# Performance work log

Measured on AMD Instinct MI355X. Metric: run time of the kernel, lower is better.

The kernel has to match this reference:

```python
import jax, jax.numpy as jnp
import numpy as np

# Hard-coded constants from the original module
GAMMA = 0.1      # self.gamma default
N_STEPS = 10     # self.n_steps default
RHO = 0.9        # RMSProp decay
LR = 0.009       # RMSProp learning rate
MOM = 0.9        # momentum
EPS = 1e-8       # RMSProp epsilon
ABS_EPS = 1e-6   # diff_abs smoothing: diff_abs(x) = sqrt(x^2 + 1e-6)

B, IN_DIM, OUT_DIM = 4096, 2048, 4096


def setup_inputs() -> dict:
    key = jax.random.key(0)
    k1, k2 = jax.random.split(key)
    inputs = jax.random.normal(k1, (B, IN_DIM), dtype=jnp.float32)
    # keras 'uniform' init: U(-0.05, 0.05), shape (output_dim, input_dim)
    W = jax.random.uniform(k2, (OUT_DIM, IN_DIM), minval=-0.05, maxval=0.05, dtype=jnp.float32)
    return {"inputs": inputs, "W": W}


def reference(inputs, W):
    batch = inputs.shape[0]
    out_dim = W.shape[0]
    a = jnp.sqrt(inputs * inputs + ABS_EPS)          # diff_abs(inputs), [B, in_dim]
    act = lambda u: 0.5 * (1.0 + jnp.exp(-u))        # self.activation

    def cost(x):
        # l1_norm.sum() + l1_inov + own_norm  (prior = 0)
        l1 = (GAMMA * act(x @ W) * a).sum()
        l1_inov = (GAMMA / 10.0) * jnp.sum(x * x)
        own = GAMMA * jnp.sum(jnp.sqrt(x * x + ABS_EPS))
        return l1 + l1_inov + own

    grad_cost = jax.grad(cost)

    def step(carry, _):
        x, acc1, acc2 = carry
        g = grad_cost(x)                              # [B, out_dim]
        new_acc1 = RHO * acc1 + (1.0 - RHO) * g * g
        denom = jnp.sqrt(new_acc1 + EPS)
        new_acc2 = MOM * acc2 - LR * g / denom
        cand = x - LR * g / denom
        t = 0.1 * LR / denom                          # elementwise prox threshold
        new_x = jnp.maximum(cand - t, 0.0) + jnp.minimum(cand + t, 0.0) + MOM * new_acc2
        new_x = jax.lax.stop_gradient(new_x)          # theano disconnected_grad
        return (new_x, new_acc1, new_acc2), None

    z = jnp.zeros((batch, out_dim), dtype=inputs.dtype)
    # scan runs n_steps; last step's l1_norm uses the state after n_steps-1 updates,
    # so run n_steps-1 updates then compute the final l1_norm directly.
    (x, _, _), _ = jax.lax.scan(step, (z, z, z), None, length=N_STEPS - 1)
    return GAMMA * act(x @ W) * a                     # outputs[-1][-1]: last l1_norm, [B, in_dim]
```

## Files before the change

### kernel.cpp

```cpp
#include <hip/hip_runtime.h>
#include <cstdint>
#include <cstddef>

#define B_DIM   4096
#define IN_DIM  2048
#define OUT_DIM 4096

typedef __attribute__((ext_vector_type(8))) __bf16 bf16x8;
typedef __attribute__((ext_vector_type(4))) float  f32x4;
typedef unsigned short ushortT;

__device__ __forceinline__ ushortT f2bf(float f) {
    unsigned int u = __float_as_uint(f);
    u += 0x7FFFu + ((u >> 16) & 1u);
    return (ushortT)(u >> 16);
}
__device__ __forceinline__ float bf2f(ushortT b) {
    return __uint_as_float(((unsigned int)b) << 16);
}

__device__ __forceinline__ void gload16(const void* g, void* l) {
    __builtin_amdgcn_global_load_lds(
        (const __attribute__((address_space(1))) void*)g,
        (__attribute__((address_space(3))) void*)l, 16, 0, 0);
}

__global__ void prep_g0_kernel(const float* __restrict__ in, ushortT* __restrict__ Gb) {
    int i = blockIdx.x * 256 + threadIdx.x;
    float4 v = reinterpret_cast<const float4*>(in)[i];
    ushort4 g;
    g.x = f2bf(-0.05f * sqrtf(v.x * v.x + 1e-6f));
    g.y = f2bf(-0.05f * sqrtf(v.y * v.y + 1e-6f));
    g.z = f2bf(-0.05f * sqrtf(v.z * v.z + 1e-6f));
    g.w = f2bf(-0.05f * sqrtf(v.w * v.w + 1e-6f));
    reinterpret_cast<ushort4*>(Gb)[i] = g;
}

__global__ void conv_w_kernel(const float* __restrict__ W, ushortT* __restrict__ Wb,
                              ushortT* __restrict__ WTb) {
    __shared__ float tile[64][65];
    const int i0 = blockIdx.x * 64;
    const int j0 = blockIdx.y * 64;
    const int c  = threadIdx.x & 63;
    const int rq = threadIdx.x >> 6;
#pragma unroll
    for (int rp = 0; rp < 16; ++rp) {
        int row = rp * 4 + rq;
        float w = W[(size_t)(j0 + row) * IN_DIM + i0 + c];
        tile[row][c] = w;
        Wb[(size_t)(j0 + row) * IN_DIM + i0 + c] = f2bf(w);
    }
    __syncthreads();
#pragma unroll
    for (int rp = 0; rp < 16; ++rp) {
        int row = rp * 4 + rq;
        WTb[(size_t)(i0 + row) * OUT_DIM + j0 + c] = f2bf(tile[c][row]);
    }
}

#define EPILOGUE(MR_)                                                          \
    float* lep = (float*)(smem + w * 4352);                                    \
    const int li = lane >> 4;                                                  \
    const int lc = lane & 15;                                                  \
    _Pragma("unroll")                                                          \
    for (int m = 0; m < (MR_); ++m) {                                          \
        _Pragma("unroll")                                                      \
        for (int n = 0; n < 4; ++n)                                            \
            _Pragma("unroll")                                                  \
            for (int i = 0; i < 4; ++i)                                        \
                lep[(li * 4 + i) * 68 + n * 16 + lc] = acc[m][n][i];           \
        asm volatile("s_waitcnt lgkmcnt(0)" ::: "memory");                     \
        __builtin_amdgcn_sched_barrier(0);                                     \
        _Pragma("unroll")                                                      \
        for (int rr = 0; rr < 4; ++rr) {                                       \
            const int row = rr + li * 4;                                       \
            float4 v = *reinterpret_cast<const float4*>(&lep[row * 68 + lc * 4]); \
            const size_t idx  = (size_t)(row0w + m * 16 + row) * N + col0w + lc * 4; \
            const size_t idx4 = idx >> 2;                                      \
            if constexpr (EPI == 0) {                                          \
                float4 iv = reinterpret_cast<const float4*>(inb)[idx4];        \
                ushort4 g;                                                     \
                g.x = f2bf(-0.05f * sqrtf(iv.x * iv.x + 1e-6f) * expf(-v.x));  \
                g.y = f2bf(-0.05f * sqrtf(iv.y * iv.y + 1e-6f) * expf(-v.y));  \
                g.z = f2bf(-0.05f * sqrtf(iv.z * iv.z + 1e-6f) * expf(-v.z));  \
                g.w = f2bf(-0.05f * sqrtf(iv.w * iv.w + 1e-6f) * expf(-v.w));  \
                *reinterpret_cast<ushort4*>(&Gb[idx]) = g;                     \
            } else if constexpr (EPI == 1) {                                   \
                float4 iv = reinterpret_cast<const float4*>(inb)[idx4];        \
                float4 o;                                                      \
                o.x = 0.05f * (1.0f + expf(-v.x)) * sqrtf(iv.x * iv.x + 1e-6f); \
                o.y = 0.05f * (1.0f + expf(-v.y)) * sqrtf(iv.y * iv.y + 1e-6f); \
                o.z = 0.05f * (1.0f + expf(-v.z)) * sqrtf(iv.z * iv.z + 1e-6f); \
                o.w = 0.05f * (1.0f + expf(-v.w)) * sqrtf(iv.w * iv.w + 1e-6f); \
                reinterpret_cast<float4*>(out)[idx4] = o;                      \
            } else {                                                           \
                ushort4 xu  = *reinterpret_cast<const ushort4*>(&xb[idx]);     \
                ushort4 a1u = *reinterpret_cast<const ushort4*>(&acc1[idx]);   \
                ushort4 a2u = *reinterpret_cast<const ushort4*>(&acc2[idx]);   \
                float xs[4] = {bf2f(xu.x), bf2f(xu.y), bf2f(xu.z), bf2f(xu.w)}; \
                float vs[4] = {v.x, v.y, v.z, v.w};                            \
                ushortT a1s[4] = {a1u.x, a1u.y, a1u.z, a1u.w};                 \
                ushortT a2s[4] = {a2u.x, a2u.y, a2u.z, a2u.w};                 \
                ushortT a1n[4], a2n[4], xbn[4];                                \
                _Pragma("unroll")                                              \
                for (int j = 0; j < 4; ++j) {                                  \
                    float g    = vs[j] + 0.02f * xs[j] + 0.1f * xs[j] * rsqrtf(xs[j] * xs[j] + 1e-6f); \
                    float a1   = 0.9f * bf2f(a1s[j]) + 0.1f * g * g;           \
                    float inv  = rsqrtf(a1 + 1e-8f);                           \
                    float r_   = 0.009f * g * inv;                             \
                    float a2   = 0.9f * bf2f(a2s[j]) - r_;                     \
                    float cand = xs[j] - r_;                                   \
                    float t_   = 0.0009f * inv;                                \
                    float xn   = fmaxf(cand - t_, 0.0f) + fminf(cand + t_, 0.0f) + 0.9f * a2; \
                    a1n[j] = f2bf(a1); a2n[j] = f2bf(a2); xbn[j] = f2bf(xn);   \
                }                                                              \
                *reinterpret_cast<ushort4*>(&acc1[idx]) = make_ushort4(a1n[0], a1n[1], a1n[2], a1n[3]); \
                *reinterpret_cast<ushort4*>(&acc2[idx]) = make_ushort4(a2n[0], a2n[1], a2n[2], a2n[3]); \
                *reinterpret_cast<ushort4*>(&xb[idx])   = make_ushort4(xbn[0], xbn[1], xbn[2], xbn[3]); \
            }                                                                  \
        }                                                                      \
        asm volatile("s_waitcnt lgkmcnt(0)" ::: "memory");                     \
    }

#define PHASE(MB, RB, SLOTP, STTILE, C0, NC)                                   \
    {                                                                          \
        const char* sb_ = (SLOTP);                                             \
        if (RB) {                                                              \
            _Pragma("unroll")                                                  \
            for (int n = 0; n < 4; ++n)                                        \
                bF[n] = *reinterpret_cast<const bf16x8*>(sb_ + bRd[n]);        \
        }                                                                      \
        bf16x8 aF[4];                                                          \
        _Pragma("unroll")                                                      \
        for (int m = 0; m < 4; ++m)                                            \
            aF[m] = *reinterpret_cast<const bf16x8*>(sb_ + aRd[m]);            \
        if ((STTILE) < nt) {                                                   \
            _Pragma("unroll")                                                  \
            for (int c = 0; c < (NC); ++c) stage_chunk((STTILE), (C0) + c);    \
        }                                                                      \
        __builtin_amdgcn_sched_barrier(0);                                     \
        __builtin_amdgcn_s_barrier();                                          \
        asm volatile("s_waitcnt lgkmcnt(0)" ::: "memory");                     \
        __builtin_amdgcn_sched_barrier(0);                                     \
        __builtin_amdgcn_s_setprio(1);                                         \
        _Pragma("unroll")                                                      \
        for (int m = 0; m < 4; ++m) {                                          \
            _Pragma("unroll")                                                  \
            for (int n = 0; n < 4; ++n)                                        \
                acc[m][n] = __builtin_amdgcn_mfma_f32_16x16x32_bf16(           \
                    aF[m], bF[n], acc[m][n], 0, 0, 0);                         \
        }                                                                      \
        __builtin_amdgcn_s_setprio(0);                                         \
        __builtin_amdgcn_s_barrier();                                          \
        __builtin_amdgcn_sched_barrier(0);                                     \
    }

template <int EPI>
__global__ __launch_bounds__(512, 1)
void gemm_phase(const ushortT* __restrict__ A, const ushortT* __restrict__ Bm,
                int N, int K,
                const float* __restrict__ inb, ushortT* __restrict__ Gb,
                float* __restrict__ out,
                ushortT* __restrict__ acc1, ushortT* __restrict__ acc2,
                ushortT* __restrict__ xb) {
    constexpr int BM = 128, BN = 256;
    constexpr int ASZ  = BM * 64;
    constexpr int SLOT = ASZ + BN * 64;
    constexpr int LA   = 1, LB = 2, L = 3;
    __shared__ alignas(16) char smem[4 * SLOT];

    const int tid  = threadIdx.x;
    const int lane = tid & 63;
    const int w    = tid >> 6;
    const int wm   = w >> 2;
    const int wn   = w & 3;
    const int nbx  = N / BN;
    const int nwg  = gridDim.x;
    const int cpx  = nwg >> 3;
    const int bid  = (int)blockIdx.x;
    const int swz  = (bid & 7) * cpx + (bid >> 3);
    const int bx   = swz % nbx;
    const int by   = swz / nbx;
    const int row0 = by * BM;
    const int col0 = bx * BN;
    const size_t strideK2 = (size_t)K * 2;

    const char* gp[L]; int lo[L];
#pragma unroll
    for (int i = 0; i < LA; ++i) {
        int Lp  = i * 512 + tid;
        int row = Lp >> 2, sl = Lp & 3;
        int src = sl ^ ((row >> 1) & 3);
        gp[i] = (const char*)A + (size_t)(row0 + row) * strideK2 + src * 16;
        lo[i] = i * 8192 + w * 1024;
    }
#pragma unroll
    for (int i = 0; i < LB; ++i) {
        int Lp  = i * 512 + tid;
        int row = Lp >> 2, sl = Lp & 3;
        int src = sl ^ ((row >> 1) & 3);
        gp[LA + i] = (const char*)Bm + (size_t)(col0 + row) * strideK2 + src * 16;
        lo[LA + i] = ASZ + i * 8192 + w * 1024;
    }
    auto stage_all = [&](int tt) {
        char* sb = smem + (tt & 3) * SLOT;
        const size_t kb = (size_t)tt * 64;
#pragma unroll
        for (int c = 0; c < L; ++c) gload16(gp[c] + kb, sb + lo[c]);
    };
    auto stage_chunk = [&](int tt, int c) {
        gload16(gp[c] + (size_t)tt * 64, smem + (tt & 3) * SLOT + lo[c]);
    };

    int aRd[4], bRd[4];
#pragma unroll
    for (int m = 0; m < 4; ++m) {
        int row = wm * 64 + m * 16 + (lane & 15);
        aRd[m] = row * 64 + (((lane >> 4) ^ ((row >> 1) & 3)) * 16);
    }
#pragma unroll
    for (int n = 0; n < 4; ++n) {
        int row = wn * 64 + n * 16 + (lane & 15);
        bRd[n] = ASZ + row * 64 + (((lane >> 4) ^ ((row >> 1) & 3)) * 16);
    }

    f32x4 acc[4][4] = {};
    const int nt = K >> 5;

    stage_all(0); stage_all(1); stage_all(2);

    for (int tt = 0; tt < nt; tt += 2) {
        if (tt + 2 < nt) asm volatile("s_waitcnt vmcnt(%0)" :: "n"(L) : "memory");
        else             asm volatile("s_waitcnt vmcnt(0)"  ::: "memory");
        __builtin_amdgcn_s_barrier();
        __builtin_amdgcn_sched_barrier(0);

        const char* sb0 = smem + (tt & 3) * SLOT;
        const char* sb1 = smem + ((tt + 1) & 3) * SLOT;
        bf16x8 bF[4];
        PHASE(0, true, sb0, tt + 3, 0, 3)
        PHASE(0, true, sb1, tt + 4, 0, 3)
    }

    __builtin_amdgcn_s_barrier();
    const int row0w = row0 + wm * 64;
    const int col0w = col0 + wn * 64;
    EPILOGUE(4)
}

template <int EPI>
__global__ __launch_bounds__(512, 4)
void gemm_mb2(const ushortT* __restrict__ A, const ushortT* __restrict__ Bm,
              int N, int K,
              const float* __restrict__ inb, ushortT* __restrict__ Gb,
              float* __restrict__ out,
              ushortT* __restrict__ acc1, ushortT* __restrict__ acc2,
              ushortT* __restrict__ xb) {
    constexpr int BM = 256, BN = 128;
    constexpr int ASZ  = BM * 64;
    constexpr int SLOT = ASZ + BN * 64;
    constexpr int CA   = 2, CB = 1, L = 3;
    __shared__ alignas(16) char smem[2 * SLOT];

    const int tid  = threadIdx.x;
    const int lane = tid & 63;
    const int w    = tid >> 6;
    const int wm   = w >> 1;
    const int wn   = w & 1;
    const int nbx  = N / BN;
    const int nwg  = gridDim.x;
    const int cpx  = nwg >> 3;
    const int bid  = (int)blockIdx.x;
    const int swz  = (bid & 7) * cpx + (bid >> 3);
    const int bx   = swz % nbx;
    const int by   = swz / nbx;
    const int row0 = by * BM;
    const int col0 = bx * BN;
    const size_t strideK2 = (size_t)K * 2;

    const char* gp[L]; int lo[L];
#pragma unroll
    for (int c = 0; c < CA; ++c) {
        int Lp  = c * 512 + tid;
        int row = Lp >> 2, sl = Lp & 3;
        int src = sl ^ ((row >> 1) & 3);
        gp[c] = (const char*)A + (size_t)(row0 + row) * strideK2 + src * 16;
        lo[c] = c * 8192 + w * 1024;
    }
#pragma unroll
    for (int c = 0; c < CB; ++c) {
        int Lp  = c * 512 + tid;
        int row = Lp >> 2, sl = Lp & 3;
        int src = sl ^ ((row >> 1) & 3);
        gp[CA + c] = (const char*)Bm + (size_t)(col0 + row) * strideK2 + src * 16;
        lo[CA + c] = ASZ + c * 8192 + w * 1024;
    }
    auto stage = [&](int tt) {
        char* sb = smem + (tt & 1) * SLOT;
        const size_t kb = (size_t)tt * 64;
#pragma unroll
        for (int c = 0; c < L; ++c) gload16(gp[c] + kb, sb + lo[c]);
    };

    int aRd[4], bRd[4];
#pragma unroll
    for (int m = 0; m < 4; ++m) {
        int row = wm * 64 + m * 16 + (lane & 15);
        aRd[m] = row * 64 + (((lane >> 4) ^ ((row >> 1) & 3)) * 16);
    }
#pragma unroll
    for (int n = 0; n < 4; ++n) {
        int row = wn * 64 + n * 16 + (lane & 15);
        bRd[n] = ASZ + row * 64 + (((lane >> 4) ^ ((row >> 1) & 3)) * 16);
    }

    f32x4 acc[4][4] = {};
    const int nt = K >> 5;

    stage(0);

    for (int tt = 0; tt < nt; ++tt) {
        asm volatile("s_waitcnt vmcnt(0)" ::: "memory");
        __builtin_amdgcn_s_barrier();
        __builtin_amdgcn_sched_barrier(0);

        const char* sb = smem + (tt & 1) * SLOT;
        bf16x8 aF[4], bF[4];
#pragma unroll
        for (int n = 0; n < 4; ++n) bF[n] = *reinterpret_cast<const bf16x8*>(sb + bRd[n]);
#pragma unroll
        for (int m = 0; m < 4; ++m) aF[m] = *reinterpret_cast<const bf16x8*>(sb + aRd[m]);
        if (tt + 1 < nt) stage(tt + 1);
        __builtin_amdgcn_s_setprio(1);
#pragma unroll
        for (int m = 0; m < 4; ++m)
#pragma unroll
            for (int n = 0; n < 4; ++n)
                acc[m][n] = __builtin_amdgcn_mfma_f32_16x16x32_bf16(aF[m], bF[n], acc[m][n], 0, 0, 0);
        __builtin_amdgcn_s_setprio(0);
    }

    __builtin_amdgcn_s_barrier();
    const int row0w = row0 + wm * 64;
    const int col0w = col0 + wn * 64;
    EPILOGUE(4)
}

extern "C" void kernel_launch(void* const* d_in, const int* in_sizes, int n_in,
                              void* d_out, int out_size, void* d_ws, size_t ws_size,
                              hipStream_t stream) {
    const float* in = (const float*)d_in[0];
    const float* W  = (const float*)d_in[1];
    float* out = (float*)d_out;
    char* ws = (char*)d_ws;

    ushortT* acc1 = (ushortT*)(ws);
    ushortT* acc2 = (ushortT*)(ws + ((size_t)32  << 20));
    ushortT* xb   = (ushortT*)(ws + ((size_t)64  << 20));
    ushortT* Wb   = (ushortT*)(ws + ((size_t)96  << 20));
    ushortT* WTb  = (ushortT*)(ws + ((size_t)112 << 20));
    ushortT* Gb   = (ushortT*)(ws + ((size_t)128 << 20));

    hipMemsetAsync(ws, 0, (size_t)96 << 20, stream);

    prep_g0_kernel<<<dim3(B_DIM * IN_DIM / 4 / 256), dim3(256), 0, stream>>>(in, Gb);
    conv_w_kernel<<<dim3(IN_DIM / 64, OUT_DIM / 64), dim3(256), 0, stream>>>(W, Wb, WTb);

    for (int step = 0; step < 9; ++step) {
        if (step > 0) {
            gemm_phase<0><<<dim3(256), dim3(512), 0, stream>>>(
                xb, WTb, IN_DIM, OUT_DIM, in, Gb, nullptr, nullptr, nullptr, nullptr);
        }
        gemm_mb2<2><<<dim3(512), dim3(512), 0, stream>>>(
            Gb, Wb, OUT_DIM, IN_DIM, nullptr, nullptr, nullptr, acc1, acc2, xb);
    }
    gemm_phase<1><<<dim3(256), dim3(512), 0, stream>>>(
        xb, WTb, IN_DIM, OUT_DIM, in, nullptr, out, nullptr, nullptr, nullptr);
}
```

Baseline: 1.576 ms.

## Triple-buffer gemm_mb K loop and precompute bf16 -0.05*|x| for epilogue

Deepens the gemm_mb shared-memory pipeline from double to triple buffering, prefetching two K tiles ahead and waiting only on the older loads so more global-to-LDS traffic stays in flight. Separately, the gradient epilogue of gemm_phase<0> now reads a precomputed bf16 array of -0.05*sqrt(x^2+eps) instead of reloading the fp32 inputs and recomputing the sqrt. This halves that epilogue's read bytes and drops a sqrt per element. The cost is a larger LDS footprint, which may limit the 4-blocks-per-CU launch bound, plus an extra 16MB buffer and slightly lower precision from the bf16 rounding of the scale factor.

```diff
diff --git a/kernel.cpp b/kernel.cpp
--- a/kernel.cpp
+++ b/kernel.cpp
@@ -25,7 +25,8 @@
         (__attribute__((address_space(3))) void*)l, 16, 0, 0);
 }
 
-__global__ void prep_g0_kernel(const float* __restrict__ in, ushortT* __restrict__ Gb) {
+__global__ void prep_g0_kernel(const float* __restrict__ in, ushortT* __restrict__ Gb,
+                               ushortT* __restrict__ negA) {
     int i = blockIdx.x * 256 + threadIdx.x;
     float4 v = reinterpret_cast<const float4*>(in)[i];
     ushort4 g;
@@ -33,7 +34,8 @@
     g.y = f2bf(-0.05f * sqrtf(v.y * v.y + 1e-6f));
     g.z = f2bf(-0.05f * sqrtf(v.z * v.z + 1e-6f));
     g.w = f2bf(-0.05f * sqrtf(v.w * v.w + 1e-6f));
-    reinterpret_cast<ushort4*>(Gb)[i] = g;
+    reinterpret_cast<ushort4*>(Gb)[i]   = g;
+    reinterpret_cast<ushort4*>(negA)[i] = g;
 }
 
 __global__ void conv_w_kernel(const float* __restrict__ W, ushortT* __restrict__ Wb,
@@ -78,12 +80,12 @@
             const size_t idx  = (size_t)(row0w + m * 16 + row) * N + col0w + lc * 4; \
             const size_t idx4 = idx >> 2;                                      \
             if constexpr (EPI == 0) {                                          \
-                float4 iv = reinterpret_cast<const float4*>(inb)[idx4];        \
+                ushort4 au = *reinterpret_cast<const ushort4*>(&nega[idx]);    \
                 ushort4 g;                                                     \
-                g.x = f2bf(-0.05f * sqrtf(iv.x * iv.x + 1e-6f) * expf(-v.x));  \
-                g.y = f2bf(-0.05f * sqrtf(iv.y * iv.y + 1e-6f) * expf(-v.y));  \
-                g.z = f2bf(-0.05f * sqrtf(iv.z * iv.z + 1e-6f) * expf(-v.z));  \
-                g.w = f2bf(-0.05f * sqrtf(iv.w * iv.w + 1e-6f) * expf(-v.w));  \
+                g.x = f2bf(bf2f(au.x) * expf(-v.x));                           \
+                g.y = f2bf(bf2f(au.y) * expf(-v.y));                           \
+                g.z = f2bf(bf2f(au.z) * expf(-v.z));                           \
+                g.w = f2bf(bf2f(au.w) * expf(-v.w));                           \
                 *reinterpret_cast<ushort4*>(&Gb[idx]) = g;                     \
             } else if constexpr (EPI == 1) {                                   \
                 float4 iv = reinterpret_cast<const float4*>(inb)[idx4];        \
@@ -159,8 +161,8 @@
 __global__ __launch_bounds__(512, 1)
 void gemm_phase(const ushortT* __restrict__ A, const ushortT* __restrict__ Bm,
                 int N, int K,
-                const float* __restrict__ inb, ushortT* __restrict__ Gb,
-                float* __restrict__ out,
+                const float* __restrict__ inb, const ushortT* __restrict__ nega,
+                ushortT* __restrict__ Gb, float* __restrict__ out,
                 ushortT* __restrict__ acc1, ushortT* __restrict__ acc2,
                 ushortT* __restrict__ xb) {
     constexpr int BM = 128, BN = 256;
@@ -250,17 +252,17 @@
 
 template <int EPI>
 __global__ __launch_bounds__(512, 4)
-void gemm_mb2(const ushortT* __restrict__ A, const ushortT* __restrict__ Bm,
-              int N, int K,
-              const float* __restrict__ inb, ushortT* __restrict__ Gb,
-              float* __restrict__ out,
-              ushortT* __restrict__ acc1, ushortT* __restrict__ acc2,
-              ushortT* __restrict__ xb) {
+void gemm_mb(const ushortT* __restrict__ A, const ushortT* __restrict__ Bm,
+             int N, int K,
+             const float* __restrict__ inb, const ushortT* __restrict__ nega,
+             ushortT* __restrict__ Gb, float* __restrict__ out,
+             ushortT* __restrict__ acc1, ushortT* __restrict__ acc2,
+             ushortT* __restrict__ xb) {
     constexpr int BM = 256, BN = 128;
     constexpr int ASZ  = BM * 64;
     constexpr int SLOT = ASZ + BN * 64;
     constexpr int CA   = 2, CB = 1, L = 3;
-    __shared__ alignas(16) char smem[2 * SLOT];
+    __shared__ alignas(16) char smem[3 * SLOT];
 
     const int tid  = threadIdx.x;
     const int lane = tid & 63;
@@ -296,7 +298,7 @@
         lo[CA + c] = ASZ + c * 8192 + w * 1024;
     }
     auto stage = [&](int tt) {
-        char* sb = smem + (tt & 1) * SLOT;
+        char* sb = smem + (tt % 3) * SLOT;
         const size_t kb = (size_t)tt * 64;
 #pragma unroll
         for (int c = 0; c < L; ++c) gload16(gp[c] + kb, sb + lo[c]);
@@ -317,20 +319,21 @@
     f32x4 acc[4][4] = {};
     const int nt = K >> 5;
 
-    stage(0);
+    stage(0); stage(1);
 
     for (int tt = 0; tt < nt; ++tt) {
-        asm volatile("s_waitcnt vmcnt(0)" ::: "memory");
+        if (tt < nt - 1) asm volatile("s_waitcnt vmcnt(%0)" :: "n"(L) : "memory");
+        else             asm volatile("s_waitcnt vmcnt(0)"  ::: "memory");
         __builtin_amdgcn_s_barrier();
         __builtin_amdgcn_sched_barrier(0);
 
-        const char* sb = smem + (tt & 1) * SLOT;
+        const char* sb = smem + (tt % 3) * SLOT;
         bf16x8 aF[4], bF[4];
 #pragma unroll
         for (int n = 0; n < 4; ++n) bF[n] = *reinterpret_cast<const bf16x8*>(sb + bRd[n]);
 #pragma unroll
         for (int m = 0; m < 4; ++m) aF[m] = *reinterpret_cast<const bf16x8*>(sb + aRd[m]);
-        if (tt + 1 < nt) stage(tt + 1);
+        if (tt + 2 < nt) stage(tt + 2);
         __builtin_amdgcn_s_setprio(1);
 #pragma unroll
         for (int m = 0; m < 4; ++m)
@@ -360,20 +363,21 @@
     ushortT* Wb   = (ushortT*)(ws + ((size_t)96  << 20));
     ushortT* WTb  = (ushortT*)(ws + ((size_t)112 << 20));
     ushortT* Gb   = (ushortT*)(ws + ((size_t)128 << 20));
+    ushortT* negA = (ushortT*)(ws + ((size_t)144 << 20));
 
     hipMemsetAsync(ws, 0, (size_t)96 << 20, stream);
 
-    prep_g0_kernel<<<dim3(B_DIM * IN_DIM / 4 / 256), dim3(256), 0, stream>>>(in, Gb);
+    prep_g0_kernel<<<dim3(B_DIM * IN_DIM / 4 / 256), dim3(256), 0, stream>>>(in, Gb, negA);
     conv_w_kernel<<<dim3(IN_DIM / 64, OUT_DIM / 64), dim3(256), 0, stream>>>(W, Wb, WTb);
 
     for (int step = 0; step < 9; ++step) {
         if (step > 0) {
             gemm_phase<0><<<dim3(256), dim3(512), 0, stream>>>(
-                xb, WTb, IN_DIM, OUT_DIM, in, Gb, nullptr, nullptr, nullptr, nullptr);
+                xb, WTb, IN_DIM, OUT_DIM, nullptr, negA, Gb, nullptr, nullptr, nullptr, nullptr);
         }
-        gemm_mb2<2><<<dim3(512), dim3(512), 0, stream>>>(
-            Gb, Wb, OUT_DIM, IN_DIM, nullptr, nullptr, nullptr, acc1, acc2, xb);
+        gemm_mb<2><<<dim3(512), dim3(512), 0, stream>>>(
+            Gb, Wb, OUT_DIM, IN_DIM, nullptr, nullptr, nullptr, nullptr, acc1, acc2, xb);
     }
     gemm_phase<1><<<dim3(256), dim3(512), 0, stream>>>(
-        xb, WTb, IN_DIM, OUT_DIM, in, nullptr, out, nullptr, nullptr, nullptr);
-}
+        xb, WTb, IN_DIM, OUT_DIM, in, nullptr, nullptr, out, nullptr, nullptr, nullptr);
+}
```

Result: no change. 1.563 ms (-0.8%).
